# Optimization experiments

Measured on AMD Instinct MI355X. Metric: run time of the kernel, lower is better.

Reference implementation:

```python
import jax, jax.numpy as jnp
import numpy as np

B, T, I, H = 512, 2048, 13, 13


def setup_inputs() -> dict:
    key = jax.random.key(0)
    ks = jax.random.split(key, 7)
    s_in = 1.0 / np.sqrt(H)
    return {
        "x": jax.random.normal(ks[0], (B, T, I), dtype=jnp.float32),
        "W_ih": jax.random.uniform(ks[1], (4 * H, I), jnp.float32, -s_in, s_in),
        "W_hh": jax.random.uniform(ks[2], (4 * H, H), jnp.float32, -s_in, s_in),
        "b_ih": jax.random.uniform(ks[3], (4 * H,), jnp.float32, -s_in, s_in),
        "b_hh": jax.random.uniform(ks[4], (4 * H,), jnp.float32, -s_in, s_in),
        "fc_w": jax.random.uniform(ks[5], (1, H), jnp.float32, -s_in, s_in),
        "fc_b": jax.random.uniform(ks[6], (1,), jnp.float32, -s_in, s_in),
    }


def _lstm(x, W_ih, W_hh, b_ih, b_hh):
    # Precompute input-to-gate projections for all timesteps: [B, T, 4H]
    xg = jnp.einsum("bti,gi->btg", x, W_ih) + b_ih + b_hh
    xg = jnp.swapaxes(xg, 0, 1)  # [T, B, 4H] for scan
    h0 = jnp.zeros((x.shape[0], H), x.dtype)
    c0 = jnp.zeros((x.shape[0], H), x.dtype)

    def step(carry, xg_t):
        h, c = carry
        gates = xg_t + h @ W_hh.T  # [B, 4H]
        i_g, f_g, g_g, o_g = jnp.split(gates, 4, axis=-1)  # PyTorch order i,f,g,o
        i_g = jax.nn.sigmoid(i_g)
        f_g = jax.nn.sigmoid(f_g)
        g_g = jnp.tanh(g_g)
        o_g = jax.nn.sigmoid(o_g)
        c_new = f_g * c + i_g * g_g
        h_new = o_g * jnp.tanh(c_new)
        return (h_new, c_new), h_new

    _, hs = jax.lax.scan(step, (h0, c0), xg)  # hs: [T, B, H]
    return jnp.swapaxes(hs, 0, 1)  # [B, T, H]


def reference(x, W_ih, W_hh, b_ih, b_hh, fc_w, fc_b):
    out = _lstm(x, W_ih, W_hh, b_ih, b_hh)  # [B, T, H]
    out = jnp.einsum("bth,oh->bto", out, fc_w) + fc_b  # [B, T, 1]
    return jax.nn.sigmoid(out)
```

## Files before the change

### kernel.cpp

```cpp
#include <hip/hip_runtime.h>
#include <hip/hip_fp16.h>

#define BB 512
#define TT 2048

typedef _Float16 half2v __attribute__((ext_vector_type(2)));

__device__ __forceinline__ float fexp2(float x){ return __builtin_amdgcn_exp2f(x); }
__device__ __forceinline__ float frcp(float x){ return __builtin_amdgcn_rcpf(x); }
__device__ __forceinline__ float sigm(float x){ return frcp(1.f + fexp2(-1.4426950408889634f*x)); }
__device__ __forceinline__ float tanhfast(float x){ return 1.f - 2.f*frcp(1.f + fexp2(2.8853900817779268f*x)); }

#define QB(v, ctrl) __int_as_float(__builtin_amdgcn_mov_dpp(__float_as_int(v), (ctrl), 0xF, 0xF, true))
#define RL(v, l)    __builtin_amdgcn_readlane((v), (l))

__global__ __launch_bounds__(256) void k_xg3(const float* __restrict__ x,
                                             const float* __restrict__ Wih,
                                             const float* __restrict__ bih,
                                             const float* __restrict__ bhh,
                                             const float* __restrict__ fcb,
                                             unsigned* __restrict__ xg_u)
{
  __shared__ float    xs[13*256];
  __shared__ unsigned ot[32*212];
  const int tid = threadIdx.x;
  const int b   = blockIdx.x >> 3;
  const int t0  = (blockIdx.x & 7) << 8;

  const float* xsrc = x + ((size_t)b*TT + t0)*13;
  #pragma unroll
  for (int it=0; it<13; ++it) xs[tid + it*256] = xsrc[tid + it*256];
  __syncthreads();

  float xv[13];
  #pragma unroll
  for (int k=0;k<13;k++) xv[k] = xs[tid*13+k];

  const int tgl = tid >> 3, u = tid & 7;
  unsigned short* otp = (unsigned short*)ot;
  #pragma unroll 2
  for (int g=0; g<52; ++g){
    float acc = bih[g] + bhh[g];
    #pragma unroll
    for (int k=0;k<13;k++) acc = fmaf(Wih[g*13+k], xv[k], acc);
    const float sc = (g>=26 && g<39) ? -2.8853900817779268f : -1.4426950408889634f;
    otp[tgl*424 + g*8 + u] = __half_as_ushort(__float2half(acc*sc));
  }
  otp[tgl*424 + 52*8 + u] =
      __half_as_ushort(__float2half(-1.4426950408889634f * fcb[0]));
  __syncthreads();

  unsigned* dst = xg_u + (size_t)b*(256*212) + (size_t)(blockIdx.x & 7)*(32*212);
  #pragma unroll
  for (int it=0; it<27; ++it){
    int i2 = tid + it*256;
    if (i2 < 32*212) dst[i2] = ot[i2];
  }
}

__global__ __launch_bounds__(64, 1) void k_rec7(const float* __restrict__ Whh,
                                                const float* __restrict__ fcw,
                                                const float* __restrict__ fcb,
                                                const unsigned short* __restrict__ xg,
                                                float* __restrict__ out)
{
  const int lane = threadIdx.x;
  const int b    = blockIdx.x;
  const int q    = lane & 3;
  const int j    = lane >> 2;
  const int jc   = (j < 13) ? j : 12;
  const int e    = (lane == 52) ? 52 : q*13 + jc;

  const float kq = (q==2) ? -2.8853900817779268f : -1.4426950408889634f;
  const float gm = (q==2) ? -5.7707801635558536f : 1.f;
  const float ga = (q==2) ?  2.8853900817779268f : 0.f;
  const float fcbias = -1.4426950408889634f * fcb[0];

  const float* wsrc = (lane == 52) ? fcw : (Whh + e*13);
  float w[13];
  #pragma unroll
  for (int k=0;k<13;k++) w[k] = wsrc[k]*kq;

  const char* gbase = (const char*)xg + (size_t)b*(256*848) + (size_t)e*16;

  float h = 0.f, c_ = 0.f;
  float hb0=0,hb1=0,hb2=0,hb3=0,hb4=0,hb5=0,hb6=0,hb7=0,hb8=0,hb9=0,hb10=0,hb11=0,hb12=0;

  float p0=0,p1=0,p2=0,p3=0,p4=0,p5=0,p6=0,p7=0;
  float* op = out + (size_t)b*TT;
  bool first = true;

#define CAPTURE(gv_, u_) do {                                                 \
    if ((u_)==1) p0=(gv_); else if ((u_)==2) p1=(gv_);                        \
    else if ((u_)==3) p2=(gv_); else if ((u_)==4) p3=(gv_);                   \
    else if ((u_)==5) p4=(gv_); else if ((u_)==6) p5=(gv_);                   \
    else if ((u_)==7) p6=(gv_);                                               \
    else { p7=(gv_);                                                          \
      if (!first){                                                            \
        if (lane == 52){                                                      \
          float4* o4 = (float4*)op;                                           \
          o4[0] = make_float4(p0,p1,p2,p3);                                   \
          o4[1] = make_float4(p4,p5,p6,p7);                                   \
        }                                                                     \
        op += 8;                                                              \
      }                                                                       \
      first = false;                                                          \
    }                                                                         \
  } while(0)

#define STEP(xv_, u_) do {                                                    \
    float dA = fmaf(w[0], hb0, (xv_));                                        \
    dA = fmaf(w[1], hb1, dA);                                                 \
    dA = fmaf(w[2], hb2, dA);                                                 \
    dA = fmaf(w[3], hb3, dA);                                                 \
    dA = fmaf(w[4], hb4, dA);                                                 \
    float dB = w[5]*hb5;                                                      \
    dB = fmaf(w[6], hb6, dB);                                                 \
    dB = fmaf(w[7], hb7, dB);                                                 \
    dB = fmaf(w[8], hb8, dB);                                                 \
    float dC = w[9]*hb9;                                                      \
    dC = fmaf(w[10], hb10, dC);                                               \
    dC = fmaf(w[11], hb11, dC);                                               \
    dC = fmaf(w[12], hb12, dC);                                               \
    float s  = (dB + dC) + dA;                                                \
    float r  = frcp(1.f + fexp2(s));                                          \
    float g  = fmaf(gm, r, ga);                                               \
    CAPTURE(g, u_);                                                           \
    float ggb = QB(g, 0xAA);                                                  \
    float gfb = QB(g, 0x55);                                                  \
    float gob = QB(g, 0xFF);                                                  \
    float go2 = gob + gob;                                                    \
    c_ = fmaf(gfb, c_, g*ggb);                                                \
    float r2 = frcp(1.f + fexp2(c_));                                         \
    h = fmaf(go2, r2, -gob);                                                  \
    int hv_ = __float_as_int(h);                                              \
    hb0  = __int_as_float(RL(hv_, 0));                                        \
    hb1  = __int_as_float(RL(hv_, 4));                                        \
    hb2  = __int_as_float(RL(hv_, 8));                                        \
    hb3  = __int_as_float(RL(hv_, 12));                                       \
    hb4  = __int_as_float(RL(hv_, 16));                                       \
    hb5  = __int_as_float(RL(hv_, 20));                                       \
    hb6  = __int_as_float(RL(hv_, 24));                                       \
    hb7  = __int_as_float(RL(hv_, 28));                                       \
    hb8  = __int_as_float(RL(hv_, 32));                                       \
    hb9  = __int_as_float(RL(hv_, 36));                                       \
    hb10 = __int_as_float(RL(hv_, 40));                                       \
    hb11 = __int_as_float(RL(hv_, 44));                                       \
    hb12 = __int_as_float(RL(hv_, 48));                                       \
  } while(0)

#define XLO(w_) (float)(__builtin_bit_cast(half2v, (w_)).x)
#define XHI(w_) (float)(__builtin_bit_cast(half2v, (w_)).y)

#define STEP8(Q) do {                                                         \
    STEP(XLO(Q.x), 0); STEP(XHI(Q.x), 1);                                     \
    STEP(XLO(Q.y), 2); STEP(XHI(Q.y), 3);                                     \
    STEP(XLO(Q.z), 4); STEP(XHI(Q.z), 5);                                     \
    STEP(XLO(Q.w), 6); STEP(XHI(Q.w), 7);                                     \
  } while(0)

  uint4 q0 = *(const uint4*)(gbase);
  uint4 q1 = *(const uint4*)(gbase + 848);
  uint4 q2 = *(const uint4*)(gbase + 2*848);
  uint4 q3 = *(const uint4*)(gbase + 3*848);

  for (int i=0; i<63; ++i){
    const char* pn = gbase + (size_t)(4*i+4)*848;
    uint4 c0 = q0; q0 = *(const uint4*)(pn);
    STEP8(c0);
    uint4 c1 = q1; q1 = *(const uint4*)(pn + 848);
    STEP8(c1);
    uint4 c2 = q2; q2 = *(const uint4*)(pn + 2*848);
    STEP8(c2);
    uint4 c3 = q3; q3 = *(const uint4*)(pn + 3*848);
    STEP8(c3);
  }
  STEP8(q0); STEP8(q1); STEP8(q2); STEP8(q3);

  {
    float s = fcbias;
    s = fmaf(w[0],  hb0,  s);
    s = fmaf(w[1],  hb1,  s);
    s = fmaf(w[2],  hb2,  s);
    s = fmaf(w[3],  hb3,  s);
    s = fmaf(w[4],  hb4,  s);
    s = fmaf(w[5],  hb5,  s);
    s = fmaf(w[6],  hb6,  s);
    s = fmaf(w[7],  hb7,  s);
    s = fmaf(w[8],  hb8,  s);
    s = fmaf(w[9],  hb9,  s);
    s = fmaf(w[10], hb10, s);
    s = fmaf(w[11], hb11, s);
    s = fmaf(w[12], hb12, s);
    float r = frcp(1.f + fexp2(s));
    if (lane == 52){
      float4* o4 = (float4*)op;
      o4[0] = make_float4(p0,p1,p2,p3);
      o4[1] = make_float4(p4,p5,p6,r);
    }
  }

#undef STEP8
#undef STEP
#undef CAPTURE
#undef XLO
#undef XHI
}

__global__ __launch_bounds__(64) void k_rec_fb(
    const float* __restrict__ x,   const float* __restrict__ Whh,
    const float* __restrict__ Wih, const float* __restrict__ bih, const float* __restrict__ bhh,
    const float* __restrict__ fcw, const float* __restrict__ fcb,
    float* __restrict__ out)
{
  const int lane = threadIdx.x;
  const int c    = lane >> 4;
  const int j    = lane & 15;
  const int b    = blockIdx.x*4 + c;
  const bool act = (j < 13);
  const int jj   = act ? j : 0;

  float whh[4][13], wih[4][13], bias[4];
  #pragma unroll
  for (int q=0;q<4;q++){
    #pragma unroll
    for (int k=0;k<13;k++){
      float w1 = Whh[(q*13+jj)*13 + k];
      float w2 = Wih[(q*13+jj)*13 + k];
      whh[q][k] = act ? w1 : 0.f;
      wih[q][k] = act ? w2 : 0.f;
    }
    bias[q] = bih[q*13+jj] + bhh[q*13+jj];
  }
  const float fcwj = act ? fcw[jj] : 0.f;
  const float fcb0 = fcb[0];

  const float* xpf = x + (size_t)b*(TT*13) + jj;
  float* op = out + (size_t)b*TT;

  float h = 0.f, cs = 0.f;
  float xsc = *xpf;

  for (int t=0; t<TT; ++t){
    float xscn = 0.f;
    if (t+1 < TT) { xpf += 13; xscn = *xpf; }

    float hb[13], xb[13];
    {
      int hbits = __float_as_int(h);
      int xbits = __float_as_int(xsc);
      #define HB(k) hb[k] = __int_as_float(__builtin_amdgcn_ds_swizzle(hbits, ((k)<<5)|0x10)); \
                    xb[k] = __int_as_float(__builtin_amdgcn_ds_swizzle(xbits, ((k)<<5)|0x10));
      HB(0) HB(1) HB(2) HB(3) HB(4) HB(5) HB(6) HB(7) HB(8) HB(9) HB(10) HB(11) HB(12)
      #undef HB
    }
    float a0 = bias[0], a1 = bias[1], a2 = bias[2], a3 = bias[3];
    #pragma unroll
    for (int k=0;k<13;k++){
      float xk = xb[k], hk = hb[k];
      a0 += wih[0][k]*xk + whh[0][k]*hk;
      a1 += wih[1][k]*xk + whh[1][k]*hk;
      a2 += wih[2][k]*xk + whh[2][k]*hk;
      a3 += wih[3][k]*xk + whh[3][k]*hk;
    }
    float ig = sigm(a0), fg = sigm(a1), gg = tanhfast(a2), og = sigm(a3);
    cs = fg*cs + ig*gg;
    h  = og * tanhfast(cs);

    float p = act ? fcwj*h : 0.f;
    #define RED(m) p += __int_as_float(__builtin_amdgcn_ds_swizzle(__float_as_int(p), ((m)<<10)|0x1F));
    RED(1) RED(2) RED(4) RED(8)
    #undef RED
    if (j == 0) op[t] = sigm(p + fcb0);
    xsc = xscn;
  }
}

extern "C" void kernel_launch(void* const* d_in, const int* in_sizes, int n_in,
                              void* d_out, int out_size, void* d_ws, size_t ws_size,
                              hipStream_t stream)
{
  const float* x   = (const float*)d_in[0];
  const float* Wih = (const float*)d_in[1];
  const float* Whh = (const float*)d_in[2];
  const float* bih = (const float*)d_in[3];
  const float* bhh = (const float*)d_in[4];
  const float* fcw = (const float*)d_in[5];
  const float* fcb = (const float*)d_in[6];
  float* out = (float*)d_out;

  const size_t XG_BYTES = (size_t)BB*256*848;

  if (ws_size >= XG_BYTES){
    unsigned* xg = (unsigned*)d_ws;
    k_xg3<<<dim3(BB*8), dim3(256), 0, stream>>>(x, Wih, bih, bhh, fcb, xg);
    k_rec7<<<dim3(BB), dim3(64), 0, stream>>>(Whh, fcw, fcb,
                                              (const unsigned short*)xg, out);
  } else {
    k_rec_fb<<<dim3(BB/4), dim3(64), 0, stream>>>(x, Whh, Wih, bih, bhh, fcw, fcb, out);
  }
}
```

Baseline: 323.2 us.

## Fuse input projection into recurrent kernel, dropping precomputed fp16 gate buffer

Removes the separate input-projection kernel and its fp16 workspace. The recurrent kernel now loads raw x for each group of 8 timesteps as float2 per lane and prefetches two groups ahead. It computes each gate's input projection inline by broadcasting x values with readlane and running 13 FMAs per step. This removes a second launch and the workspace write and read, and keeps fp32 precision for the input projection. The cost is 13 extra readlanes and FMAs on the serial per-timestep critical path.

```diff
diff --git a/kernel.cpp b/kernel.cpp
--- a/kernel.cpp
+++ b/kernel.cpp
@@ -1,87 +1,53 @@
 #include <hip/hip_runtime.h>
-#include <hip/hip_fp16.h>
 
 #define BB 512
 #define TT 2048
 
-typedef _Float16 half2v __attribute__((ext_vector_type(2)));
-
 __device__ __forceinline__ float fexp2(float x){ return __builtin_amdgcn_exp2f(x); }
 __device__ __forceinline__ float frcp(float x){ return __builtin_amdgcn_rcpf(x); }
-__device__ __forceinline__ float sigm(float x){ return frcp(1.f + fexp2(-1.4426950408889634f*x)); }
-__device__ __forceinline__ float tanhfast(float x){ return 1.f - 2.f*frcp(1.f + fexp2(2.8853900817779268f*x)); }
 
 #define QB(v, ctrl) __int_as_float(__builtin_amdgcn_mov_dpp(__float_as_int(v), (ctrl), 0xF, 0xF, true))
 #define RL(v, l)    __builtin_amdgcn_readlane((v), (l))
 
-__global__ __launch_bounds__(256) void k_xg3(const float* __restrict__ x,
-                                             const float* __restrict__ Wih,
-                                             const float* __restrict__ bih,
-                                             const float* __restrict__ bhh,
-                                             const float* __restrict__ fcb,
-                                             unsigned* __restrict__ xg_u)
-{
-  __shared__ float    xs[13*256];
-  __shared__ unsigned ot[32*212];
-  const int tid = threadIdx.x;
-  const int b   = blockIdx.x >> 3;
-  const int t0  = (blockIdx.x & 7) << 8;
-
-  const float* xsrc = x + ((size_t)b*TT + t0)*13;
-  #pragma unroll
-  for (int it=0; it<13; ++it) xs[tid + it*256] = xsrc[tid + it*256];
-  __syncthreads();
-
-  float xv[13];
-  #pragma unroll
-  for (int k=0;k<13;k++) xv[k] = xs[tid*13+k];
-
-  const int tgl = tid >> 3, u = tid & 7;
-  unsigned short* otp = (unsigned short*)ot;
-  #pragma unroll 2
-  for (int g=0; g<52; ++g){
-    float acc = bih[g] + bhh[g];
-    #pragma unroll
-    for (int k=0;k<13;k++) acc = fmaf(Wih[g*13+k], xv[k], acc);
-    const float sc = (g>=26 && g<39) ? -2.8853900817779268f : -1.4426950408889634f;
-    otp[tgl*424 + g*8 + u] = __half_as_ushort(__float2half(acc*sc));
-  }
-  otp[tgl*424 + 52*8 + u] =
-      __half_as_ushort(__float2half(-1.4426950408889634f * fcb[0]));
-  __syncthreads();
-
-  unsigned* dst = xg_u + (size_t)b*(256*212) + (size_t)(blockIdx.x & 7)*(32*212);
-  #pragma unroll
-  for (int it=0; it<27; ++it){
-    int i2 = tid + it*256;
-    if (i2 < 32*212) dst[i2] = ot[i2];
-  }
-}
-
-__global__ __launch_bounds__(64, 1) void k_rec7(const float* __restrict__ Whh,
-                                                const float* __restrict__ fcw,
-                                                const float* __restrict__ fcb,
-                                                const unsigned short* __restrict__ xg,
-                                                float* __restrict__ out)
+__global__ __launch_bounds__(64, 1) void k_rec_f(
+    const float* __restrict__ x,
+    const float* __restrict__ Wih,
+    const float* __restrict__ Whh,
+    const float* __restrict__ bih,
+    const float* __restrict__ bhh,
+    const float* __restrict__ fcw,
+    const float* __restrict__ fcb,
+    float* __restrict__ out)
 {
   const int lane = threadIdx.x;
   const int b    = blockIdx.x;
   const int q    = lane & 3;
   const int j    = lane >> 2;
   const int jc   = (j < 13) ? j : 12;
-  const int e    = (lane == 52) ? 52 : q*13 + jc;
+  const bool fcl = (lane == 52);
+  const int e    = fcl ? 0 : q*13 + jc;
 
   const float kq = (q==2) ? -2.8853900817779268f : -1.4426950408889634f;
   const float gm = (q==2) ? -5.7707801635558536f : 1.f;
   const float ga = (q==2) ?  2.8853900817779268f : 0.f;
   const float fcbias = -1.4426950408889634f * fcb[0];
 
-  const float* wsrc = (lane == 52) ? fcw : (Whh + e*13);
-  float w[13];
+  const float* wsrc = fcl ? fcw : (Whh + e*13);
+  const float  kx   = fcl ? 0.f : kq;
+
+  float w[13], wx[13];
   #pragma unroll
-  for (int k=0;k<13;k++) w[k] = wsrc[k]*kq;
+  for (int k=0;k<13;k++) w[k]  = wsrc[k]*kq;
+  #pragma unroll
+  for (int k=0;k<13;k++) wx[k] = Wih[e*13+k]*kx;
 
-  const char* gbase = (const char*)xg + (size_t)b*(256*848) + (size_t)e*16;
+  const float biass = fcl ? fcbias : (bih[e]+bhh[e])*kq;
+
+  const float* xb = x + (size_t)b*(TT*13);
+  const int ll = (lane < 52) ? lane : 51;
+
+  float2 xcur = ((const float2*)(xb      ))[ll];
+  float2 xnxt = ((const float2*)(xb + 104))[ll];
 
   float h = 0.f, c_ = 0.f;
   float hb0=0,hb1=0,hb2=0,hb3=0,hb4=0,hb5=0,hb6=0,hb7=0,hb8=0,hb9=0,hb10=0,hb11=0,hb12=0;
@@ -149,33 +115,24 @@
     hb12 = __int_as_float(RL(hv_, 48));                                       \
   } while(0)
 
-#define XLO(w_) (float)(__builtin_bit_cast(half2v, (w_)).x)
-#define XHI(w_) (float)(__builtin_bit_cast(half2v, (w_)).y)
-
-#define STEP8(Q) do {                                                         \
-    STEP(XLO(Q.x), 0); STEP(XHI(Q.x), 1);                                     \
-    STEP(XLO(Q.y), 2); STEP(XHI(Q.y), 3);                                     \
-    STEP(XLO(Q.z), 4); STEP(XHI(Q.z), 5);                                     \
-    STEP(XLO(Q.w), 6); STEP(XHI(Q.w), 7);                                     \
+#define STEPX(u_) do {                                                        \
+    float sx_ = biass;                                                        \
+    _Pragma("unroll")                                                         \
+    for (int k_ = 0; k_ < 13; ++k_){                                          \
+      const int f_ = (u_)*13 + k_;                                            \
+      float xe_ = (f_ & 1) ? xcur.y : xcur.x;                                 \
+      sx_ = fmaf(wx[k_], __int_as_float(RL(__float_as_int(xe_), f_>>1)), sx_);\
+    }                                                                         \
+    STEP(sx_, u_);                                                            \
   } while(0)
 
-  uint4 q0 = *(const uint4*)(gbase);
-  uint4 q1 = *(const uint4*)(gbase + 848);
-  uint4 q2 = *(const uint4*)(gbase + 2*848);
-  uint4 q3 = *(const uint4*)(gbase + 3*848);
-
-  for (int i=0; i<63; ++i){
-    const char* pn = gbase + (size_t)(4*i+4)*848;
-    uint4 c0 = q0; q0 = *(const uint4*)(pn);
-    STEP8(c0);
-    uint4 c1 = q1; q1 = *(const uint4*)(pn + 848);
-    STEP8(c1);
-    uint4 c2 = q2; q2 = *(const uint4*)(pn + 2*848);
-    STEP8(c2);
-    uint4 c3 = q3; q3 = *(const uint4*)(pn + 3*848);
-    STEP8(c3);
+  for (int g=0; g<256; ++g){
+    const int gn = (g+2 < 256) ? (g+2) : 255;
+    float2 xfut = ((const float2*)(xb + (size_t)gn*104))[ll];
+    STEPX(0); STEPX(1); STEPX(2); STEPX(3);
+    STEPX(4); STEPX(5); STEPX(6); STEPX(7);
+    xcur = xnxt; xnxt = xfut;
   }
-  STEP8(q0); STEP8(q1); STEP8(q2); STEP8(q3);
 
   {
     float s = fcbias;
@@ -200,80 +157,9 @@
     }
   }
 
-#undef STEP8
+#undef STEPX
 #undef STEP
 #undef CAPTURE
-#undef XLO
-#undef XHI
-}
-
-__global__ __launch_bounds__(64) void k_rec_fb(
-    const float* __restrict__ x,   const float* __restrict__ Whh,
-    const float* __restrict__ Wih, const float* __restrict__ bih, const float* __restrict__ bhh,
-    const float* __restrict__ fcw, const float* __restrict__ fcb,
-    float* __restrict__ out)
-{
-  const int lane = threadIdx.x;
-  const int c    = lane >> 4;
-  const int j    = lane & 15;
-  const int b    = blockIdx.x*4 + c;
-  const bool act = (j < 13);
-  const int jj   = act ? j : 0;
-
-  float whh[4][13], wih[4][13], bias[4];
-  #pragma unroll
-  for (int q=0;q<4;q++){
-    #pragma unroll
-    for (int k=0;k<13;k++){
-      float w1 = Whh[(q*13+jj)*13 + k];
-      float w2 = Wih[(q*13+jj)*13 + k];
-      whh[q][k] = act ? w1 : 0.f;
-      wih[q][k] = act ? w2 : 0.f;
-    }
-    bias[q] = bih[q*13+jj] + bhh[q*13+jj];
-  }
-  const float fcwj = act ? fcw[jj] : 0.f;
-  const float fcb0 = fcb[0];
-
-  const float* xpf = x + (size_t)b*(TT*13) + jj;
-  float* op = out + (size_t)b*TT;
-
-  float h = 0.f, cs = 0.f;
-  float xsc = *xpf;
-
-  for (int t=0; t<TT; ++t){
-    float xscn = 0.f;
-    if (t+1 < TT) { xpf += 13; xscn = *xpf; }
-
-    float hb[13], xb[13];
-    {
-      int hbits = __float_as_int(h);
-      int xbits = __float_as_int(xsc);
-      #define HB(k) hb[k] = __int_as_float(__builtin_amdgcn_ds_swizzle(hbits, ((k)<<5)|0x10)); \
-                    xb[k] = __int_as_float(__builtin_amdgcn_ds_swizzle(xbits, ((k)<<5)|0x10));
-      HB(0) HB(1) HB(2) HB(3) HB(4) HB(5) HB(6) HB(7) HB(8) HB(9) HB(10) HB(11) HB(12)
-      #undef HB
-    }
-    float a0 = bias[0], a1 = bias[1], a2 = bias[2], a3 = bias[3];
-    #pragma unroll
-    for (int k=0;k<13;k++){
-      float xk = xb[k], hk = hb[k];
-      a0 += wih[0][k]*xk + whh[0][k]*hk;
-      a1 += wih[1][k]*xk + whh[1][k]*hk;
-      a2 += wih[2][k]*xk + whh[2][k]*hk;
-      a3 += wih[3][k]*xk + whh[3][k]*hk;
-    }
-    float ig = sigm(a0), fg = sigm(a1), gg = tanhfast(a2), og = sigm(a3);
-    cs = fg*cs + ig*gg;
-    h  = og * tanhfast(cs);
-
-    float p = act ? fcwj*h : 0.f;
-    #define RED(m) p += __int_as_float(__builtin_amdgcn_ds_swizzle(__float_as_int(p), ((m)<<10)|0x1F));
-    RED(1) RED(2) RED(4) RED(8)
-    #undef RED
-    if (j == 0) op[t] = sigm(p + fcb0);
-    xsc = xscn;
-  }
 }
 
 extern "C" void kernel_launch(void* const* d_in, const int* in_sizes, int n_in,
@@ -289,14 +175,6 @@
   const float* fcb = (const float*)d_in[6];
   float* out = (float*)d_out;
 
-  const size_t XG_BYTES = (size_t)BB*256*848;
-
-  if (ws_size >= XG_BYTES){
-    unsigned* xg = (unsigned*)d_ws;
-    k_xg3<<<dim3(BB*8), dim3(256), 0, stream>>>(x, Wih, bih, bhh, fcb, xg);
-    k_rec7<<<dim3(BB), dim3(64), 0, stream>>>(Whh, fcw, fcb,
-                                              (const unsigned short*)xg, out);
-  } else {
-    k_rec_fb<<<dim3(BB/4), dim3(64), 0, stream>>>(x, Whh, Wih, bih, bhh, fcw, fcb, out);
-  }
+  (void)d_ws; (void)ws_size;
+  k_rec_f<<<dim3(BB), dim3(64), 0, stream>>>(x, Wih, Whh, bih, bhh, fcw, fcb, out);
 }
```

Result: slower. 380.9 us (+17.8%).

## Interleave two batch recurrences per wavefront to hide serial latency

Applied to the files above, without the earlier changes.

The recurrence kernel now processes two batch rows per 64-lane block, alternating timestep updates for each so their independent dependency chains overlap in one wave. The grid is halved accordingly and prefetch depth per sequence is reduced from four to two vectors. This trades fewer concurrent waves per CU for more instruction-level parallelism within each wave, and raises register pressure.

```diff
diff --git a/kernel.cpp b/kernel.cpp
--- a/kernel.cpp
+++ b/kernel.cpp
@@ -58,14 +58,15 @@
   }
 }
 
-__global__ __launch_bounds__(64, 1) void k_rec7(const float* __restrict__ Whh,
+__global__ __launch_bounds__(64, 1) void k_rec8(const float* __restrict__ Whh,
                                                 const float* __restrict__ fcw,
                                                 const float* __restrict__ fcb,
                                                 const unsigned short* __restrict__ xg,
                                                 float* __restrict__ out)
 {
   const int lane = threadIdx.x;
-  const int b    = blockIdx.x;
+  const int b0   = blockIdx.x*2;
+  const int b1   = b0 + 1;
   const int q    = lane & 3;
   const int j    = lane >> 2;
   const int jc   = (j < 13) ? j : 12;
@@ -81,126 +82,152 @@
   #pragma unroll
   for (int k=0;k<13;k++) w[k] = wsrc[k]*kq;
 
-  const char* gbase = (const char*)xg + (size_t)b*(256*848) + (size_t)e*16;
-
-  float h = 0.f, c_ = 0.f;
-  float hb0=0,hb1=0,hb2=0,hb3=0,hb4=0,hb5=0,hb6=0,hb7=0,hb8=0,hb9=0,hb10=0,hb11=0,hb12=0;
-
-  float p0=0,p1=0,p2=0,p3=0,p4=0,p5=0,p6=0,p7=0;
-  float* op = out + (size_t)b*TT;
-  bool first = true;
-
-#define CAPTURE(gv_, u_) do {                                                 \
-    if ((u_)==1) p0=(gv_); else if ((u_)==2) p1=(gv_);                        \
-    else if ((u_)==3) p2=(gv_); else if ((u_)==4) p3=(gv_);                   \
-    else if ((u_)==5) p4=(gv_); else if ((u_)==6) p5=(gv_);                   \
-    else if ((u_)==7) p6=(gv_);                                               \
-    else { p7=(gv_);                                                          \
-      if (!first){                                                            \
+  const char* gbaseA = (const char*)xg + (size_t)b0*(256*848) + (size_t)e*16;
+  const char* gbaseB = (const char*)xg + (size_t)b1*(256*848) + (size_t)e*16;
+
+  float hA = 0.f, cA_ = 0.f, hB = 0.f, cB_ = 0.f;
+  float hbA0=0,hbA1=0,hbA2=0,hbA3=0,hbA4=0,hbA5=0,hbA6=0,hbA7=0,hbA8=0,hbA9=0,hbA10=0,hbA11=0,hbA12=0;
+  float hbB0=0,hbB1=0,hbB2=0,hbB3=0,hbB4=0,hbB5=0,hbB6=0,hbB7=0,hbB8=0,hbB9=0,hbB10=0,hbB11=0,hbB12=0;
+
+  float pA0=0,pA1=0,pA2=0,pA3=0,pA4=0,pA5=0,pA6=0,pA7=0;
+  float pB0=0,pB1=0,pB2=0,pB3=0,pB4=0,pB5=0,pB6=0,pB7=0;
+  float* opA = out + (size_t)b0*TT;
+  float* opB = out + (size_t)b1*TT;
+  bool firstA = true, firstB = true;
+
+#define CAPTURE(S, gv_, u_) do {                                              \
+    if ((u_)==1) p##S##0=(gv_); else if ((u_)==2) p##S##1=(gv_);              \
+    else if ((u_)==3) p##S##2=(gv_); else if ((u_)==4) p##S##3=(gv_);         \
+    else if ((u_)==5) p##S##4=(gv_); else if ((u_)==6) p##S##5=(gv_);         \
+    else if ((u_)==7) p##S##6=(gv_);                                          \
+    else { p##S##7=(gv_);                                                     \
+      if (!first##S){                                                         \
         if (lane == 52){                                                      \
-          float4* o4 = (float4*)op;                                           \
-          o4[0] = make_float4(p0,p1,p2,p3);                                   \
-          o4[1] = make_float4(p4,p5,p6,p7);                                   \
+          float4* o4 = (float4*)op##S;                                        \
+          o4[0] = make_float4(p##S##0,p##S##1,p##S##2,p##S##3);               \
+          o4[1] = make_float4(p##S##4,p##S##5,p##S##6,p##S##7);               \
         }                                                                     \
-        op += 8;                                                              \
+        op##S += 8;                                                           \
       }                                                                       \
-      first = false;                                                          \
+      first##S = false;                                                       \
     }                                                                         \
   } while(0)
 
-#define STEP(xv_, u_) do {                                                    \
-    float dA = fmaf(w[0], hb0, (xv_));                                        \
-    dA = fmaf(w[1], hb1, dA);                                                 \
-    dA = fmaf(w[2], hb2, dA);                                                 \
-    dA = fmaf(w[3], hb3, dA);                                                 \
-    dA = fmaf(w[4], hb4, dA);                                                 \
-    float dB = w[5]*hb5;                                                      \
-    dB = fmaf(w[6], hb6, dB);                                                 \
-    dB = fmaf(w[7], hb7, dB);                                                 \
-    dB = fmaf(w[8], hb8, dB);                                                 \
-    float dC = w[9]*hb9;                                                      \
-    dC = fmaf(w[10], hb10, dC);                                               \
-    dC = fmaf(w[11], hb11, dC);                                               \
-    dC = fmaf(w[12], hb12, dC);                                               \
+#define STEP(S, xv_, u_) do {                                                 \
+    float dA = fmaf(w[0], hb##S##0, (xv_));                                   \
+    dA = fmaf(w[1], hb##S##1, dA);                                            \
+    dA = fmaf(w[2], hb##S##2, dA);                                            \
+    dA = fmaf(w[3], hb##S##3, dA);                                            \
+    dA = fmaf(w[4], hb##S##4, dA);                                            \
+    float dB = w[5]*hb##S##5;                                                 \
+    dB = fmaf(w[6], hb##S##6, dB);                                            \
+    dB = fmaf(w[7], hb##S##7, dB);                                            \
+    dB = fmaf(w[8], hb##S##8, dB);                                            \
+    float dC = w[9]*hb##S##9;                                                 \
+    dC = fmaf(w[10], hb##S##10, dC);                                          \
+    dC = fmaf(w[11], hb##S##11, dC);                                          \
+    dC = fmaf(w[12], hb##S##12, dC);                                          \
     float s  = (dB + dC) + dA;                                                \
     float r  = frcp(1.f + fexp2(s));                                          \
     float g  = fmaf(gm, r, ga);                                               \
-    CAPTURE(g, u_);                                                           \
+    CAPTURE(S, g, u_);                                                        \
     float ggb = QB(g, 0xAA);                                                  \
     float gfb = QB(g, 0x55);                                                  \
     float gob = QB(g, 0xFF);                                                  \
     float go2 = gob + gob;                                                    \
-    c_ = fmaf(gfb, c_, g*ggb);                                                \
-    float r2 = frcp(1.f + fexp2(c_));                                         \
-    h = fmaf(go2, r2, -gob);                                                  \
-    int hv_ = __float_as_int(h);                                              \
-    hb0  = __int_as_float(RL(hv_, 0));                                        \
-    hb1  = __int_as_float(RL(hv_, 4));                                        \
-    hb2  = __int_as_float(RL(hv_, 8));                                        \
-    hb3  = __int_as_float(RL(hv_, 12));                                       \
-    hb4  = __int_as_float(RL(hv_, 16));                                       \
-    hb5  = __int_as_float(RL(hv_, 20));                                       \
-    hb6  = __int_as_float(RL(hv_, 24));                                       \
-    hb7  = __int_as_float(RL(hv_, 28));                                       \
-    hb8  = __int_as_float(RL(hv_, 32));                                       \
-    hb9  = __int_as_float(RL(hv_, 36));                                       \
-    hb10 = __int_as_float(RL(hv_, 40));                                       \
-    hb11 = __int_as_float(RL(hv_, 44));                                       \
-    hb12 = __int_as_float(RL(hv_, 48));                                       \
+    c##S##_ = fmaf(gfb, c##S##_, g*ggb);                                      \
+    float r2 = frcp(1.f + fexp2(c##S##_));                                    \
+    h##S = fmaf(go2, r2, -gob);                                               \
+    int hv_ = __float_as_int(h##S);                                           \
+    hb##S##0  = __int_as_float(RL(hv_, 0));                                   \
+    hb##S##1  = __int_as_float(RL(hv_, 4));                                   \
+    hb##S##2  = __int_as_float(RL(hv_, 8));                                   \
+    hb##S##3  = __int_as_float(RL(hv_, 12));                                  \
+    hb##S##4  = __int_as_float(RL(hv_, 16));                                  \
+    hb##S##5  = __int_as_float(RL(hv_, 20));                                  \
+    hb##S##6  = __int_as_float(RL(hv_, 24));                                  \
+    hb##S##7  = __int_as_float(RL(hv_, 28));                                  \
+    hb##S##8  = __int_as_float(RL(hv_, 32));                                  \
+    hb##S##9  = __int_as_float(RL(hv_, 36));                                  \
+    hb##S##10 = __int_as_float(RL(hv_, 40));                                  \
+    hb##S##11 = __int_as_float(RL(hv_, 44));                                  \
+    hb##S##12 = __int_as_float(RL(hv_, 48));                                  \
   } while(0)
 
 #define XLO(w_) (float)(__builtin_bit_cast(half2v, (w_)).x)
 #define XHI(w_) (float)(__builtin_bit_cast(half2v, (w_)).y)
 
-#define STEP8(Q) do {                                                         \
-    STEP(XLO(Q.x), 0); STEP(XHI(Q.x), 1);                                     \
-    STEP(XLO(Q.y), 2); STEP(XHI(Q.y), 3);                                     \
-    STEP(XLO(Q.z), 4); STEP(XHI(Q.z), 5);                                     \
-    STEP(XLO(Q.w), 6); STEP(XHI(Q.w), 7);                                     \
+#define STEP8PAIR(QA, QB) do {                                                \
+    STEP(A, XLO(QA.x), 0); STEP(B, XLO(QB.x), 0);                             \
+    STEP(A, XHI(QA.x), 1); STEP(B, XHI(QB.x), 1);                             \
+    STEP(A, XLO(QA.y), 2); STEP(B, XLO(QB.y), 2);                             \
+    STEP(A, XHI(QA.y), 3); STEP(B, XHI(QB.y), 3);                             \
+    STEP(A, XLO(QA.z), 4); STEP(B, XLO(QB.z), 4);                             \
+    STEP(A, XHI(QA.z), 5); STEP(B, XHI(QB.z), 5);                             \
+    STEP(A, XLO(QA.w), 6); STEP(B, XLO(QB.w), 6);                             \
+    STEP(A, XHI(QA.w), 7); STEP(B, XHI(QB.w), 7);                             \
   } while(0)
 
-  uint4 q0 = *(const uint4*)(gbase);
-  uint4 q1 = *(const uint4*)(gbase + 848);
-  uint4 q2 = *(const uint4*)(gbase + 2*848);
-  uint4 q3 = *(const uint4*)(gbase + 3*848);
-
-  for (int i=0; i<63; ++i){
-    const char* pn = gbase + (size_t)(4*i+4)*848;
-    uint4 c0 = q0; q0 = *(const uint4*)(pn);
-    STEP8(c0);
-    uint4 c1 = q1; q1 = *(const uint4*)(pn + 848);
-    STEP8(c1);
-    uint4 c2 = q2; q2 = *(const uint4*)(pn + 2*848);
-    STEP8(c2);
-    uint4 c3 = q3; q3 = *(const uint4*)(pn + 3*848);
-    STEP8(c3);
-  }
-  STEP8(q0); STEP8(q1); STEP8(q2); STEP8(q3);
+  uint4 qA0 = *(const uint4*)(gbaseA);
+  uint4 qA1 = *(const uint4*)(gbaseA + 848);
+  uint4 qB0 = *(const uint4*)(gbaseB);
+  uint4 qB1 = *(const uint4*)(gbaseB + 848);
+
+  for (int i=0; i<127; ++i){
+    const char* pA = gbaseA + (size_t)(2*i+2)*848;
+    const char* pB = gbaseB + (size_t)(2*i+2)*848;
+    uint4 cA = qA0; qA0 = *(const uint4*)(pA);
+    uint4 cB = qB0; qB0 = *(const uint4*)(pB);
+    STEP8PAIR(cA, cB);
+    cA = qA1; qA1 = *(const uint4*)(pA + 848);
+    cB = qB1; qB1 = *(const uint4*)(pB + 848);
+    STEP8PAIR(cA, cB);
+  }
+  STEP8PAIR(qA0, qB0);
+  STEP8PAIR(qA1, qB1);
 
   {
-    float s = fcbias;
-    s = fmaf(w[0],  hb0,  s);
-    s = fmaf(w[1],  hb1,  s);
-    s = fmaf(w[2],  hb2,  s);
-    s = fmaf(w[3],  hb3,  s);
-    s = fmaf(w[4],  hb4,  s);
-    s = fmaf(w[5],  hb5,  s);
-    s = fmaf(w[6],  hb6,  s);
-    s = fmaf(w[7],  hb7,  s);
-    s = fmaf(w[8],  hb8,  s);
-    s = fmaf(w[9],  hb9,  s);
-    s = fmaf(w[10], hb10, s);
-    s = fmaf(w[11], hb11, s);
-    s = fmaf(w[12], hb12, s);
-    float r = frcp(1.f + fexp2(s));
+    float sA = fcbias;
+    sA = fmaf(w[0],  hbA0,  sA);
+    sA = fmaf(w[1],  hbA1,  sA);
+    sA = fmaf(w[2],  hbA2,  sA);
+    sA = fmaf(w[3],  hbA3,  sA);
+    sA = fmaf(w[4],  hbA4,  sA);
+    sA = fmaf(w[5],  hbA5,  sA);
+    sA = fmaf(w[6],  hbA6,  sA);
+    sA = fmaf(w[7],  hbA7,  sA);
+    sA = fmaf(w[8],  hbA8,  sA);
+    sA = fmaf(w[9],  hbA9,  sA);
+    sA = fmaf(w[10], hbA10, sA);
+    sA = fmaf(w[11], hbA11, sA);
+    sA = fmaf(w[12], hbA12, sA);
+    float rA = frcp(1.f + fexp2(sA));
+    float sB = fcbias;
+    sB = fmaf(w[0],  hbB0,  sB);
+    sB = fmaf(w[1],  hbB1,  sB);
+    sB = fmaf(w[2],  hbB2,  sB);
+    sB = fmaf(w[3],  hbB3,  sB);
+    sB = fmaf(w[4],  hbB4,  sB);
+    sB = fmaf(w[5],  hbB5,  sB);
+    sB = fmaf(w[6],  hbB6,  sB);
+    sB = fmaf(w[7],  hbB7,  sB);
+    sB = fmaf(w[8],  hbB8,  sB);
+    sB = fmaf(w[9],  hbB9,  sB);
+    sB = fmaf(w[10], hbB10, sB);
+    sB = fmaf(w[11], hbB11, sB);
+    sB = fmaf(w[12], hbB12, sB);
+    float rB = frcp(1.f + fexp2(sB));
     if (lane == 52){
-      float4* o4 = (float4*)op;
-      o4[0] = make_float4(p0,p1,p2,p3);
-      o4[1] = make_float4(p4,p5,p6,r);
+      float4* o4 = (float4*)opA;
+      o4[0] = make_float4(pA0,pA1,pA2,pA3);
+      o4[1] = make_float4(pA4,pA5,pA6,rA);
+      o4 = (float4*)opB;
+      o4[0] = make_float4(pB0,pB1,pB2,pB3);
+      o4[1] = make_float4(pB4,pB5,pB6,rB);
     }
   }
 
-#undef STEP8
+#undef STEP8PAIR
 #undef STEP
 #undef CAPTURE
 #undef XLO
@@ -294,8 +321,8 @@
   if (ws_size >= XG_BYTES){
     unsigned* xg = (unsigned*)d_ws;
     k_xg3<<<dim3(BB*8), dim3(256), 0, stream>>>(x, Wih, bih, bhh, fcb, xg);
-    k_rec7<<<dim3(BB), dim3(64), 0, stream>>>(Whh, fcw, fcb,
-                                              (const unsigned short*)xg, out);
+    k_rec8<<<dim3(BB/2), dim3(64), 0, stream>>>(Whh, fcw, fcb,
+                                                (const unsigned short*)xg, out);
   } else {
     k_rec_fb<<<dim3(BB/4), dim3(64), 0, stream>>>(x, Whh, Wih, bih, bhh, fcw, fcb, out);
   }
```

New measurement: 496.5 us. 1.54x slower.
